# Performance work log

Measured on AMD Instinct MI355X. Metric: run time of the kernel, lower is better.

Reference implementation:

```python
import jax, jax.numpy as jnp
import numpy as np

NR, NL, K, TOPK, C, B = 4096, 16384, 8, 10, 16, 4
W_OCC, W_MDN, W_INT = 0.2, 1.0, 0.1
LOG2PI = float(np.log(2.0 * np.pi))


def setup_inputs() -> dict:
    key = jax.random.key(0)
    ks = jax.random.split(key, 12)
    radar_indices = jnp.concatenate([
        jax.random.randint(ks[0], (NR, 1), 0, B),
        jax.random.randint(ks[1], (NR, 1), 0, 41),
        jax.random.randint(ks[2], (NR, 2), 0, 176),
    ], axis=1).astype(jnp.int32)
    lidar_indices = jnp.concatenate([
        jax.random.randint(ks[3], (NL, 1), 0, B),
        jax.random.randint(ks[4], (NL, 1), 0, 41),
        jax.random.randint(ks[5], (NL, 2), 0, 176),
    ], axis=1).astype(jnp.int32)
    return {
        'mu_off': jax.random.normal(ks[6], (NR, K, 3)) * 2.0,
        'log_sig_off': jax.random.normal(ks[7], (NR, K, 3)) * 0.3,
        'mu_int': jax.random.normal(ks[8], (NR, K, 1)),
        'occ_logit': jax.random.normal(ks[9], (NR, K, 1)),
        'mix_logit': jax.random.normal(ks[10], (NR, K, 1)),
        'lidar_features': jax.random.normal(ks[11], (NL, C)),
        'radar_indices': radar_indices,
        'lidar_indices': lidar_indices,
        'gt_topk': TOPK,
    }


def _match(radar_indices, lidar_indices, topk):
    # per-batch top-k nearest lidar voxels for each radar voxel (vectorized:
    # dense masked distance matrix replaces the per-batch python loop)
    rb, lb = radar_indices[:, 0], lidar_indices[:, 0]
    rpos = radar_indices[:, 1:].astype(jnp.float32)  # (Nr,3) zyx
    lpos = lidar_indices[:, 1:].astype(jnp.float32)  # (Nl,3)
    d2 = ((rpos * rpos).sum(-1)[:, None] + (lpos * lpos).sum(-1)[None, :]
          - 2.0 * (rpos @ lpos.T))  # (Nr,Nl) squared dist, same order as cdist
    same = rb[:, None] == lb[None, :]
    d2 = jnp.where(same, d2, jnp.inf)  # cross-batch pairs excluded
    _, nn_idx = jax.lax.top_k(-d2, topk)  # (Nr,topk) smallest distances
    matched = same.any(axis=1)  # (Nr,)
    offs_zyx = (lidar_indices[nn_idx, 1:]
                - radar_indices[:, None, 1:]).astype(jnp.float32)  # (Nr,topk,3)
    offs_zyx = jnp.where(matched[:, None, None], offs_zyx, 0.0)
    return matched, nn_idx, offs_zyx


def reference(mu_off, log_sig_off, mu_int, occ_logit, mix_logit,
              lidar_features, radar_indices, lidar_indices, gt_topk):
    matched, nn_idx, offs_zyx = _match(radar_indices, lidar_indices, gt_topk)
    gt_feat = jnp.where(matched[:, None, None], lidar_features[nn_idx], 0.0)  # (Nr,T,C)
    y = offs_zyx[..., ::-1]  # flip zyx -> xyz, (Nr,T,3)

    # occupancy BCE-with-logits against matched mask
    occ_any = occ_logit[..., 0].max(axis=1)  # (Nr,)
    tgt = matched.astype(occ_any.dtype)
    occ_loss = (tgt * jax.nn.softplus(-occ_any)
                + (1.0 - tgt) * jax.nn.softplus(occ_any)).mean()

    # MDN log-prob: (Nr,T,K) mixture components
    log_pi = jax.nn.log_softmax(mix_logit[..., 0], axis=1)  # (Nr,K)
    mu_ = mu_off[:, None, :, :]       # (Nr,1,K,3)
    ls_ = log_sig_off[:, None, :, :]
    sigma2 = jnp.exp(2.0 * ls_) + 1e-12
    y_ = y[:, :, None, :]             # (Nr,T,1,3)
    logN = -0.5 * (((y_ - mu_) ** 2) / sigma2 + 2.0 * ls_ + LOG2PI).sum(-1)  # (Nr,T,K)
    log_post = logN + log_pi[:, None, :]
    logp = jax.nn.logsumexp(log_post, axis=-1)  # (Nr,T)

    # masked means emulate boolean-index-then-mean over matched rows
    m = matched.astype(jnp.float32)
    cnt = m.sum()
    T = logp.shape[1]
    mdn_nll = -(logp * m[:, None]).sum() / (cnt * T)

    # intensity loss (C % 4 == 0 path)
    gt_int = gt_feat.reshape(gt_feat.shape[0], gt_feat.shape[1], C // 4, 4)[..., 3].mean(axis=2)  # (Nr,T)
    r = jax.nn.softmax(log_post, axis=-1)  # (Nr,T,K) responsibilities
    term = r * jnp.abs(mu_int[:, None, :, 0] - gt_int[:, :, None])  # (Nr,T,K)
    int_loss = (term * m[:, None, None]).sum() / (cnt * T * r.shape[-1])

    return W_OCC * occ_loss + W_MDN * mdn_nll + W_INT * int_loss
```

## Files before the change

kernel.cpp:

```cpp
#include <hip/hip_runtime.h>
#include <cstdint>

#define NRAD 4096
#define NLID 16384
#define KMIX 8
#define TOPK 10
#define CF   16
#define LOG2PI 1.8378770664093453f

static constexpr unsigned INF_D2 = 62851u;

__device__ __forceinline__ void insert_key(unsigned (&t)[TOPK], unsigned key) {
#pragma unroll
    for (int i = TOPK - 1; i >= 1; --i) {
        unsigned hi = key > t[i - 1] ? key : t[i - 1];
        t[i] = hi < t[i] ? hi : t[i];
    }
    t[0] = key < t[0] ? key : t[0];
}

__device__ __forceinline__ void merge10(unsigned (&t)[TOPK], int lane,
                                        unsigned& mine, unsigned& first, unsigned& tenth) {
#pragma unroll
    for (int r = 0; r < TOPK; ++r) {
        unsigned v = t[0];
#pragma unroll
        for (int off = 32; off >= 1; off >>= 1) {
            unsigned o = __shfl_xor(v, off, 64);
            v = o < v ? o : v;
        }
        if (t[0] == v) {
#pragma unroll
            for (int i = 0; i < TOPK - 1; ++i) t[i] = t[i + 1];
            t[TOPK - 1] = 0xFFFFFFFFu;
        }
        if (lane == r) mine = v;
        if (r == 0) first = v;
        if (r == TOPK - 1) tenth = v;
    }
}

__device__ __forceinline__ float waveReduceSum(float v) {
#pragma unroll
    for (int off = 32; off >= 1; off >>= 1) v += __shfl_down(v, off, 64);
    return v;
}

__global__ __launch_bounds__(256) void prep_kernel(
        const int* __restrict__ lidar_indices,
        unsigned* __restrict__ packed_full,
        uint2* __restrict__ compacted,
        int* __restrict__ cursor) {
    int i = blockIdx.x * 256 + threadIdx.x;
    int lane = threadIdx.x & 63;
    int4 li = ((const int4*)lidar_indices)[i];
    int b = li.x;
    unsigned pos = ((unsigned)li.y << 16) | ((unsigned)li.z << 8) | (unsigned)li.w;
    packed_full[i] = ((unsigned)b << 22) | pos;
#pragma unroll
    for (int b2 = 0; b2 < 4; ++b2) {
        unsigned long long mask = __ballot(b == b2);
        if (b == b2) {
            int leader = __ffsll(mask) - 1;
            int off = (int)__popcll(mask & ((1ull << lane) - 1ull));
            int s = 0;
            if (lane == leader) s = atomicAdd(&cursor[b2], (int)__popcll(mask));
            s = __shfl(s, leader, 64);
            compacted[b2 * NLID + s + off] = make_uint2(pos, (unsigned)i);
        }
    }
}

__global__ __launch_bounds__(256) void topk_kernel(
        const uint2* __restrict__ compacted,
        const unsigned* __restrict__ packed_full,
        const int* __restrict__ cursor,
        const int* __restrict__ radar_indices,
        int* __restrict__ nn_out, int* __restrict__ matched_out) {
    int lane = threadIdx.x & 63;
    int row  = blockIdx.x * 4 + (threadIdx.x >> 6);
    int4 ri = ((const int4*)radar_indices)[row];
    int rb = ri.x, rz = ri.y, ry = ri.z, rx = ri.w;
    int c_cnt = cursor[rb];

    unsigned t[TOPK];
#pragma unroll
    for (int i = 0; i < TOPK; ++i) t[i] = 0xFFFFFFFFu;

    const uint4* src = (const uint4*)(compacted + rb * NLID);
    int iters = (c_cnt + 127) >> 7;
    uint4 q = src[lane];
    for (int it = 0; it < iters; ++it) {
        uint4 qn = q;
        if (it + 1 < iters) qn = src[(it + 1) * 64 + lane];
        int c0 = (it * 64 + lane) * 2;
        {
            int dz = (int)((q.x >> 16) & 63u)  - rz;
            int dy = (int)((q.x >> 8)  & 255u) - ry;
            int dx = (int)(q.x & 255u)         - rx;
            unsigned d2 = (unsigned)(dz * dz + dy * dy + dx * dx);
            unsigned key = (c0 < c_cnt) ? ((d2 << 14) | q.y) : 0xFFFFFFFFu;
            if (key < t[TOPK - 1]) insert_key(t, key);
        }
        {
            int dz = (int)((q.z >> 16) & 63u)  - rz;
            int dy = (int)((q.z >> 8)  & 255u) - ry;
            int dx = (int)(q.z & 255u)         - rx;
            unsigned d2 = (unsigned)(dz * dz + dy * dy + dx * dx);
            unsigned key = (c0 + 1 < c_cnt) ? ((d2 << 14) | q.w) : 0xFFFFFFFFu;
            if (key < t[TOPK - 1]) insert_key(t, key);
        }
        q = qn;
    }

    unsigned mine = 0, first = 0, tenth = 0;
    merge10(t, lane, mine, first, tenth);
    bool matched = true;

    if (tenth == 0xFFFFFFFFu) {
#pragma unroll
        for (int i = 0; i < TOPK; ++i) t[i] = 0xFFFFFFFFu;
        for (int it = 0; it < NLID / 256; ++it) {
            uint4 p4 = ((const uint4*)packed_full)[it * 64 + lane];
            unsigned base = it * 256 + lane * 4;
            unsigned ps[4] = {p4.x, p4.y, p4.z, p4.w};
#pragma unroll
            for (int j = 0; j < 4; ++j) {
                unsigned p = ps[j];
                int b  = (int)(p >> 22);
                int dz = (int)((p >> 16) & 63u)  - rz;
                int dy = (int)((p >> 8)  & 255u) - ry;
                int dx = (int)(p & 255u)         - rx;
                unsigned d2 = (unsigned)(dz * dz + dy * dy + dx * dx);
                unsigned hi = (b == rb) ? d2 : INF_D2;
                insert_key(t, (hi << 14) | (base + j));
            }
        }
        merge10(t, lane, mine, first, tenth);
        matched = first < (INF_D2 << 14);
    }

    if (lane < TOPK) nn_out[row * TOPK + lane] = (int)(mine & 0x3FFFu);
    if (lane == 0)   matched_out[row] = matched ? 1 : 0;
}

__global__ __launch_bounds__(256) void mdn_kernel(
        const float* __restrict__ mu_off, const float* __restrict__ log_sig_off,
        const float* __restrict__ mu_int, const float* __restrict__ occ_logit,
        const float* __restrict__ mix_logit, const float* __restrict__ lidar_features,
        const int* __restrict__ radar_indices, const int* __restrict__ lidar_indices,
        const int* __restrict__ nn, const int* __restrict__ matched,
        float* __restrict__ accum,
        unsigned* __restrict__ dctr,
        float* __restrict__ out) {
    int gid = blockIdx.x * 256 + threadIdx.x;
    int n  = gid / TOPK;
    int tt = gid - n * TOPK;
    int m  = matched[n];
    float mf = (float)m;
    int nni = nn[gid];

    int4 ri = ((const int4*)radar_indices)[n];
    int4 li = ((const int4*)lidar_indices)[nni];
    float y0 = mf * (float)(li.w - ri.w);
    float y1 = mf * (float)(li.z - ri.z);
    float y2 = mf * (float)(li.y - ri.y);

    float mix[KMIX];
    float mmax = -1e30f;
#pragma unroll
    for (int k = 0; k < KMIX; ++k) {
        mix[k] = mix_logit[n * KMIX + k];
        mmax = fmaxf(mmax, mix[k]);
    }
    float msum = 0.f;
#pragma unroll
    for (int k = 0; k < KMIX; ++k) msum += expf(mix[k] - mmax);
    float logZ = mmax + logf(msum);

    float lpost[KMIX];
    float pmax = -1e30f;
#pragma unroll
    for (int k = 0; k < KMIX; ++k) {
        int bidx = (n * KMIX + k) * 3;
        float mu0 = mu_off[bidx + 0], mu1 = mu_off[bidx + 1], mu2 = mu_off[bidx + 2];
        float l0 = log_sig_off[bidx + 0], l1 = log_sig_off[bidx + 1], l2 = log_sig_off[bidx + 2];
        float s0 = expf(2.f * l0) + 1e-12f;
        float s1 = expf(2.f * l1) + 1e-12f;
        float s2 = expf(2.f * l2) + 1e-12f;
        float d0 = y0 - mu0, d1 = y1 - mu1, d2v = y2 - mu2;
        float q = d0 * d0 / s0 + d1 * d1 / s1 + d2v * d2v / s2
                + 2.f * (l0 + l1 + l2) + 3.f * LOG2PI;
        lpost[k] = -0.5f * q + (mix[k] - logZ);
        pmax = fmaxf(pmax, lpost[k]);
    }
    float ex[KMIX];
    float se = 0.f;
#pragma unroll
    for (int k = 0; k < KMIX; ++k) { ex[k] = expf(lpost[k] - pmax); se += ex[k]; }
    float logp = pmax + logf(se);

    float gt = 0.f;
    if (m) {
        const float* lf = lidar_features + nni * CF;
        gt = 0.25f * (lf[3] + lf[7] + lf[11] + lf[15]);
    }
    float inv_se = 1.f / se;
    float isum = 0.f;
#pragma unroll
    for (int k = 0; k < KMIX; ++k)
        isum += ex[k] * inv_se * fabsf(mu_int[n * KMIX + k] - gt);

    float lp = mf * logp;
    float ip = mf * isum;
    float oc = 0.f, mc = 0.f;
    if (tt == 0) {
        float oa = -1e30f;
#pragma unroll
        for (int k = 0; k < KMIX; ++k) oa = fmaxf(oa, occ_logit[n * KMIX + k]);
        float soft_abs = log1pf(expf(-fabsf(oa)));
        oc = mf * (soft_abs + fmaxf(-oa, 0.f)) + (1.f - mf) * (soft_abs + fmaxf(oa, 0.f));
        mc = mf;
    }

    lp = waveReduceSum(lp); ip = waveReduceSum(ip);
    oc = waveReduceSum(oc); mc = waveReduceSum(mc);
    __shared__ float sA[4], sB[4], sC[4], sD[4];
    int wid = threadIdx.x >> 6, lane = threadIdx.x & 63;
    if (lane == 0) { sA[wid] = lp; sB[wid] = ip; sC[wid] = oc; sD[wid] = mc; }
    __syncthreads();
    if (threadIdx.x == 0) {
        atomicAdd(&accum[0], sA[0] + sA[1] + sA[2] + sA[3]);
        atomicAdd(&accum[1], sB[0] + sB[1] + sB[2] + sB[3]);
        atomicAdd(&accum[2], sC[0] + sC[1] + sC[2] + sC[3]);
        atomicAdd(&accum[3], sD[0] + sD[1] + sD[2] + sD[3]);
        __threadfence();
        unsigned done = atomicAdd(dctr, 1u);
        if (done == gridDim.x - 1) {
            __threadfence();
            float a = __hip_atomic_load(&accum[0], __ATOMIC_RELAXED, __HIP_MEMORY_SCOPE_AGENT);
            float b = __hip_atomic_load(&accum[1], __ATOMIC_RELAXED, __HIP_MEMORY_SCOPE_AGENT);
            float c = __hip_atomic_load(&accum[2], __ATOMIC_RELAXED, __HIP_MEMORY_SCOPE_AGENT);
            float d = __hip_atomic_load(&accum[3], __ATOMIC_RELAXED, __HIP_MEMORY_SCOPE_AGENT);
            float occ_loss = c / (float)NRAD;
            float mdn_nll  = -a / (d * (float)TOPK);
            float int_loss = b / (d * (float)TOPK * (float)KMIX);
            out[0] = 0.2f * occ_loss + mdn_nll + 0.1f * int_loss;
        }
    }
}

extern "C" void kernel_launch(void* const* d_in, const int* in_sizes, int n_in,
                              void* d_out, int out_size, void* d_ws, size_t ws_size,
                              hipStream_t stream) {
    const float* mu_off         = (const float*)d_in[0];
    const float* log_sig_off    = (const float*)d_in[1];
    const float* mu_int         = (const float*)d_in[2];
    const float* occ_logit      = (const float*)d_in[3];
    const float* mix_logit      = (const float*)d_in[4];
    const float* lidar_features = (const float*)d_in[5];
    const int*   radar_indices  = (const int*)d_in[6];
    const int*   lidar_indices  = (const int*)d_in[7];
    float* out = (float*)d_out;

    char* ws = (char*)d_ws;
    unsigned* packed_full = (unsigned*)(ws + 0);
    uint2*    compacted   = (uint2*)(ws + 65536);
    int*      cursor      = (int*)(ws + 589824);
    float*    accum       = (float*)(ws + 589840);
    unsigned* dctr        = (unsigned*)(ws + 589856);
    int*      nn          = (int*)(ws + 589888);
    int*      matched     = (int*)(ws + 753728);

    hipMemsetAsync(ws + 589824, 0, 64, stream);

    hipLaunchKernelGGL(prep_kernel, dim3(NLID / 256), dim3(256), 0, stream,
                       lidar_indices, packed_full, compacted, cursor);
    hipLaunchKernelGGL(topk_kernel, dim3(NRAD / 4), dim3(256), 0, stream,
                       compacted, packed_full, cursor, radar_indices, nn, matched);
    hipLaunchKernelGGL(mdn_kernel, dim3(NRAD * TOPK / 256), dim3(256), 0, stream,
                       mu_off, log_sig_off, mu_int, occ_logit, mix_logit,
                       lidar_features, radar_indices, lidar_indices,
                       nn, matched, accum, dctr, out);
}
```

Baseline: 122.8 us.

## Bin radar rows by batch in a per-batch prep kernel and drop memset

The prep kernel now runs one 1024-thread block per batch. Each block compacts the lidar points and radar rows of its batch using shared-memory cursors, and it zeroes the accumulators itself, so the separate memset is no longer needed. The top-k kernel reads radar rows in batch-sorted order, so the waves in a block scan the same compacted lidar segment, which should improve cache reuse and even out the loop trip counts. It also uses __mul24 for the distance products. The cost is that prep runs on only 4 blocks, serialising 16K lidar reads per block, which may lengthen that stage.

Measured after the change: 121.3 us. About the same (-1.2%).

```diff
diff --git a/kernel.cpp b/kernel.cpp
--- a/kernel.cpp
+++ b/kernel.cpp
@@ -46,42 +46,75 @@
     return v;
 }
 
-__global__ __launch_bounds__(256) void prep_kernel(
+__global__ __launch_bounds__(1024) void prep_kernel(
         const int* __restrict__ lidar_indices,
+        const int* __restrict__ radar_indices,
         unsigned* __restrict__ packed_full,
         uint2* __restrict__ compacted,
-        int* __restrict__ cursor) {
-    int i = blockIdx.x * 256 + threadIdx.x;
-    int lane = threadIdx.x & 63;
-    int4 li = ((const int4*)lidar_indices)[i];
-    int b = li.x;
-    unsigned pos = ((unsigned)li.y << 16) | ((unsigned)li.z << 8) | (unsigned)li.w;
-    packed_full[i] = ((unsigned)b << 22) | pos;
-#pragma unroll
-    for (int b2 = 0; b2 < 4; ++b2) {
-        unsigned long long mask = __ballot(b == b2);
-        if (b == b2) {
+        int* __restrict__ rbin,
+        int* __restrict__ ctrl) {
+    __shared__ int lcur, rcur;
+    int tid = threadIdx.x, lane = tid & 63, myb = blockIdx.x;
+    if (tid == 0) { lcur = 0; rcur = 0; }
+    __syncthreads();
+
+#pragma unroll
+    for (int it = 0; it < NLID / 1024; ++it) {
+        int i = it * 1024 + tid;
+        int4 li = ((const int4*)lidar_indices)[i];
+        unsigned pos = ((unsigned)li.y << 16) | ((unsigned)li.z << 8) | (unsigned)li.w;
+        bool mine = (li.x == myb);
+        if (mine) packed_full[i] = ((unsigned)li.x << 22) | pos;
+        unsigned long long mask = __ballot(mine);
+        if (mine) {
             int leader = __ffsll(mask) - 1;
             int off = (int)__popcll(mask & ((1ull << lane) - 1ull));
             int s = 0;
-            if (lane == leader) s = atomicAdd(&cursor[b2], (int)__popcll(mask));
+            if (lane == leader) s = atomicAdd(&lcur, (int)__popcll(mask));
             s = __shfl(s, leader, 64);
-            compacted[b2 * NLID + s + off] = make_uint2(pos, (unsigned)i);
-        }
-    }
+            compacted[myb * NLID + s + off] = make_uint2(pos, (unsigned)i);
+        }
+    }
+
+#pragma unroll
+    for (int it = 0; it < NRAD / 1024; ++it) {
+        int r = it * 1024 + tid;
+        int rb = radar_indices[r * 4];
+        bool mine = (rb == myb);
+        unsigned long long mask = __ballot(mine);
+        if (mine) {
+            int leader = __ffsll(mask) - 1;
+            int off = (int)__popcll(mask & ((1ull << lane) - 1ull));
+            int s = 0;
+            if (lane == leader) s = atomicAdd(&rcur, (int)__popcll(mask));
+            s = __shfl(s, leader, 64);
+            rbin[myb * NRAD + s + off] = r;
+        }
+    }
+
+    __syncthreads();
+    if (tid == 0) { ctrl[myb] = lcur; ctrl[12 + myb] = rcur; }
+    if (myb == 0 && tid >= 64 && tid < 69) ctrl[4 + (tid - 64)] = 0;
 }
 
 __global__ __launch_bounds__(256) void topk_kernel(
         const uint2* __restrict__ compacted,
         const unsigned* __restrict__ packed_full,
-        const int* __restrict__ cursor,
+        const int* __restrict__ ctrl,
+        const int* __restrict__ rbin,
         const int* __restrict__ radar_indices,
         int* __restrict__ nn_out, int* __restrict__ matched_out) {
     int lane = threadIdx.x & 63;
-    int row  = blockIdx.x * 4 + (threadIdx.x >> 6);
+    int g = blockIdx.x * 4 + (threadIdx.x >> 6);
+    int r0 = ctrl[12], r1 = ctrl[13], r2 = ctrl[14];
+    int cum1 = r0, cum2 = r0 + r1, cum3 = cum2 + r2;
+    int gb = (g >= cum1) + (g >= cum2) + (g >= cum3);
+    int gbase = gb == 0 ? 0 : (gb == 1 ? cum1 : (gb == 2 ? cum2 : cum3));
+    int row = rbin[gb * NRAD + (g - gbase)];
+
     int4 ri = ((const int4*)radar_indices)[row];
     int rb = ri.x, rz = ri.y, ry = ri.z, rx = ri.w;
-    int c_cnt = cursor[rb];
+    int c_cnt = ctrl[rb];
 
     unsigned t[TOPK];
 #pragma unroll
@@ -98,7 +131,7 @@
             int dz = (int)((q.x >> 16) & 63u)  - rz;
             int dy = (int)((q.x >> 8)  & 255u) - ry;
             int dx = (int)(q.x & 255u)         - rx;
-            unsigned d2 = (unsigned)(dz * dz + dy * dy + dx * dx);
+            unsigned d2 = (unsigned)(__mul24(dz, dz) + __mul24(dy, dy) + __mul24(dx, dx));
             unsigned key = (c0 < c_cnt) ? ((d2 << 14) | q.y) : 0xFFFFFFFFu;
             if (key < t[TOPK - 1]) insert_key(t, key);
         }
@@ -106,7 +139,7 @@
             int dz = (int)((q.z >> 16) & 63u)  - rz;
             int dy = (int)((q.z >> 8)  & 255u) - ry;
             int dx = (int)(q.z & 255u)         - rx;
-            unsigned d2 = (unsigned)(dz * dz + dy * dy + dx * dx);
+            unsigned d2 = (unsigned)(__mul24(dz, dz) + __mul24(dy, dy) + __mul24(dx, dx));
             unsigned key = (c0 + 1 < c_cnt) ? ((d2 << 14) | q.w) : 0xFFFFFFFFu;
             if (key < t[TOPK - 1]) insert_key(t, key);
         }
@@ -131,7 +164,7 @@
                 int dz = (int)((p >> 16) & 63u)  - rz;
                 int dy = (int)((p >> 8)  & 255u) - ry;
                 int dx = (int)(p & 255u)         - rx;
-                unsigned d2 = (unsigned)(dz * dz + dy * dy + dx * dx);
+                unsigned d2 = (unsigned)(__mul24(dz, dz) + __mul24(dy, dy) + __mul24(dx, dx));
                 unsigned hi = (b == rb) ? d2 : INF_D2;
                 insert_key(t, (hi << 14) | (base + j));
             }
@@ -266,18 +299,18 @@
     char* ws = (char*)d_ws;
     unsigned* packed_full = (unsigned*)(ws + 0);
     uint2*    compacted   = (uint2*)(ws + 65536);
-    int*      cursor      = (int*)(ws + 589824);
-    float*    accum       = (float*)(ws + 589840);
-    unsigned* dctr        = (unsigned*)(ws + 589856);
+    int*      ctrl        = (int*)(ws + 589824);
     int*      nn          = (int*)(ws + 589888);
     int*      matched     = (int*)(ws + 753728);
-
-    hipMemsetAsync(ws + 589824, 0, 64, stream);
-
-    hipLaunchKernelGGL(prep_kernel, dim3(NLID / 256), dim3(256), 0, stream,
-                       lidar_indices, packed_full, compacted, cursor);
+    int*      rbin        = (int*)(ws + 770112);
+
+    float*    accum = (float*)(ctrl + 4);
+    unsigned* dctr  = (unsigned*)(ctrl + 8);
+
+    hipLaunchKernelGGL(prep_kernel, dim3(4), dim3(1024), 0, stream,
+                       lidar_indices, radar_indices, packed_full, compacted, rbin, ctrl);
     hipLaunchKernelGGL(topk_kernel, dim3(NRAD / 4), dim3(256), 0, stream,
-                       compacted, packed_full, cursor, radar_indices, nn, matched);
+                       compacted, packed_full, ctrl, rbin, radar_indices, nn, matched);
     hipLaunchKernelGGL(mdn_kernel, dim3(NRAD * TOPK / 256), dim3(256), 0, stream,
                        mu_off, log_sig_off, mu_int, occ_logit, mix_logit,
                        lidar_features, radar_indices, lidar_indices,
```
